# Kernel optimization log

Measured on AMD Instinct MI355X. Metric: run time of the kernel, lower is better.

## Reference

```python
import jax, jax.numpy as jnp
import numpy as np
from jax import lax

B, H_IMG, W_IMG = 512, 812, 40
HID = 128
NUM_CLASSES = 12
LSTM_IN = 32 * ((W_IMG - 5) // 2 + 1)  # 32 channels * 18 = 576


def setup_inputs() -> dict:
    key = jax.random.key(0)
    ks = jax.random.split(key, 20)
    s = 0.05
    inp = {
        "x": jax.random.normal(ks[0], (B, 1, H_IMG, W_IMG), jnp.float32),
        "conv_w": jax.random.normal(ks[1], (32, 1, 20, 5), jnp.float32) * s,
        "conv_b": jax.random.normal(ks[2], (32,), jnp.float32) * s,
        "Wih0": jax.random.normal(ks[3], (4 * HID, LSTM_IN), jnp.float32) * s,
        "Whh0": jax.random.normal(ks[4], (4 * HID, HID), jnp.float32) * s,
        "bih0": jax.random.normal(ks[5], (4 * HID,), jnp.float32) * s,
        "bhh0": jax.random.normal(ks[6], (4 * HID,), jnp.float32) * s,
        "Wih1": jax.random.normal(ks[7], (4 * HID, HID), jnp.float32) * s,
        "Whh1": jax.random.normal(ks[8], (4 * HID, HID), jnp.float32) * s,
        "bih1": jax.random.normal(ks[9], (4 * HID,), jnp.float32) * s,
        "bhh1": jax.random.normal(ks[10], (4 * HID,), jnp.float32) * s,
        "W_att": jax.random.normal(ks[11], (HID, HID), jnp.float32) * s,
        "b_att": jax.random.normal(ks[12], (HID,), jnp.float32) * s,
        "v_att": jax.random.normal(ks[13], (HID,), jnp.float32) * s,
        "W1": jax.random.normal(ks[14], (64, HID), jnp.float32) * s,
        "b1": jax.random.normal(ks[15], (64,), jnp.float32) * s,
        "W2": jax.random.normal(ks[16], (NUM_CLASSES, 64), jnp.float32) * s,
        "b2": jax.random.normal(ks[17], (NUM_CLASSES,), jnp.float32) * s,
    }
    return inp


def _lstm_layer(seq, Wih, Whh, bih, bhh):
    # seq: (T, B, I); PyTorch gate order i, f, g, o
    T, Bn, _ = seq.shape
    Hd = Whh.shape[1]
    x_proj = jnp.einsum('tbi,gi->tbg', seq, Wih) + bih + bhh  # (T,B,4H)

    def step(carry, xg):
        h, c = carry
        g = xg + h @ Whh.T
        i, f, gg, o = jnp.split(g, 4, axis=-1)
        c = jax.nn.sigmoid(f) * c + jax.nn.sigmoid(i) * jnp.tanh(gg)
        h = jax.nn.sigmoid(o) * jnp.tanh(c)
        return (h, c), h

    init = (jnp.zeros((Bn, Hd), seq.dtype), jnp.zeros((Bn, Hd), seq.dtype))
    _, hs = lax.scan(step, init, x_proj)
    return hs  # (T,B,H)


def _forward(x, conv_w, conv_b, Wih0, Whh0, bih0, bhh0, Wih1, Whh1, bih1, bhh1,
             W_att, b_att, v_att, W1, b1, W2, b2):
    # Conv2d(1->32, k=(20,5), s=(8,2)) + ReLU
    y = lax.conv_general_dilated(x, conv_w, (8, 2), 'VALID',
                                 dimension_numbers=('NCHW', 'OIHW', 'NCHW'))
    y = jax.nn.relu(y + conv_b[None, :, None, None])  # (B,32,T,W')
    b, c, t, w = y.shape
    # permute(0,2,3,1).view(b,t,-1).permute(1,0,2) -> (T,B,W'*32)
    seq = jnp.transpose(y, (2, 0, 3, 1)).reshape(t, b, w * c)
    # 2-layer LSTM (inter-layer dropout=0.2 inactive at eval)
    h1 = _lstm_layer(seq, Wih0, Whh0, bih0, bhh0)
    h2 = _lstm_layer(h1, Wih1, Whh1, bih1, bhh1)
    # additive attention pooling over time
    squish = jnp.tanh(jnp.einsum('tbh,hk->tbk', h2, W_att) + b_att)  # (T,B,H)
    attn = jnp.einsum('tbh,h->tb', squish, v_att)                     # (T,B)
    w_att_n = jax.nn.softmax(attn, axis=0)                            # softmax over T
    pooled = jnp.einsum('tb,tbh->bh', w_att_n, h2)                    # (B,H)
    # dnn1 -> (dropout inactive at eval) -> output
    hdn = pooled @ W1.T + b1
    return hdn @ W2.T + b2  # (B,num_classes)


def reference(x, conv_w, conv_b, Wih0, Whh0, bih0, bhh0, Wih1, Whh1, bih1, bhh1,
              W_att, b_att, v_att, W1, b1, W2, b2):
    return _forward(x, conv_w, conv_b, Wih0, Whh0, bih0, bhh0, Wih1, Whh1,
                    bih1, bhh1, W_att, b_att, v_att, W1, b1, W2, b2)
```

## Files before the change

kernel.cpp:

```cpp
#include <hip/hip_runtime.h>
#include <stdint.h>


#define T_STEPS 100
#define BATCH   512
#define HIDD    128
#define GATES   512
#define LSTMIN  576
#define HIMG    812
#define WIMG    40

typedef __attribute__((ext_vector_type(8))) short bf16x8;
typedef __attribute__((ext_vector_type(4))) float f32x4;
typedef __attribute__((ext_vector_type(2))) __fp16 f16x2;

__device__ inline unsigned short f2bf(float f) {
  unsigned u = __float_as_uint(f);
  unsigned r = (u + 0x7fffu + ((u >> 16) & 1u)) >> 16;
  return (unsigned short)r;
}
__device__ inline float bf2f(unsigned short b) {
  return __uint_as_float(((unsigned)b) << 16);
}
__device__ inline float fsigm(float x) {
  float e = __expf(-x);
  return __builtin_amdgcn_rcpf(1.f + e);
}
__device__ inline float ftanh(float x) {
  float e = __expf(2.f * x);
  return (e - 1.f) * __builtin_amdgcn_rcpf(e + 1.f);
}
__device__ inline void lds_barrier() {
  asm volatile("s_waitcnt lgkmcnt(0)" ::: "memory");
  __builtin_amdgcn_s_barrier();
}

__global__ void prep_kernel(const float* __restrict__ Wih0, const float* __restrict__ Whh0,
                            const float* __restrict__ Wih1, const float* __restrict__ Whh1,
                            const float* __restrict__ Watt, const float* __restrict__ convw,
                            const float* __restrict__ bih0, const float* __restrict__ bhh0,
                            const float* __restrict__ bih1, const float* __restrict__ bhh1,
                            unsigned short* __restrict__ wih0b, unsigned short* __restrict__ whh0b,
                            unsigned short* __restrict__ wih1b, unsigned short* __restrict__ whh1b,
                            unsigned short* __restrict__ wattb, f16x2* __restrict__ wpair,
                            float* __restrict__ bias0, float* __restrict__ bias1) {
  int tid = blockIdx.x * blockDim.x + threadIdx.x;
  int stride = gridDim.x * blockDim.x;
  for (int i = tid; i < GATES * LSTMIN; i += stride) wih0b[i] = f2bf(Wih0[i]);
  for (int i = tid; i < GATES * HIDD; i += stride) whh0b[i] = f2bf(Whh0[i]);
  for (int i = tid; i < GATES * HIDD; i += stride) wih1b[i] = f2bf(Wih1[i]);
  for (int i = tid; i < GATES * HIDD; i += stride) whh1b[i] = f2bf(Whh1[i]);
  for (int i = tid; i < HIDD * HIDD; i += stride) {
    int j = i >> 7, k = i & 127;
    wattb[i] = f2bf(Watt[k * HIDD + j]);
  }
  for (int i = tid; i < 50 * 32; i += stride) {
    int k2 = i >> 5, c = i & 31;
    int kh2 = k2 / 5, kw = k2 % 5;
    float lo = convw[c * 100 + (2 * kh2) * 5 + kw];
    float hi = convw[c * 100 + (2 * kh2 + 1) * 5 + kw];
    wpair[i] = __builtin_amdgcn_cvt_pkrtz(lo, hi);
  }
  for (int i = tid; i < GATES; i += stride) bias0[i] = bih0[i] + bhh0[i];
  for (int i = tid; i < GATES; i += stride) bias1[i] = bih1[i] + bhh1[i];
}

__global__ __launch_bounds__(256) void conv_kernel(const float* __restrict__ x,
                                                   const f16x2* __restrict__ wpair,
                                                   const float* __restrict__ convb,
                                                   unsigned short* __restrict__ seq) {
  __shared__ f16x2 imgp[106 * WIMG];
  const int b = blockIdx.x;
  const int chunk = blockIdx.y;
  const int t0 = chunk * 25;
  const float* src = x + (size_t)b * (HIMG * WIMG) + (size_t)(8 * t0) * WIMG;
  for (int i = threadIdx.x; i < 106 * WIMG; i += 256) {
    int r2 = i / WIMG, c = i % WIMG;
    float lo = src[(2 * r2) * WIMG + c];
    float hi = src[(2 * r2 + 1) * WIMG + c];
    imgp[i] = __builtin_amdgcn_cvt_pkrtz(lo, hi);
  }
  __syncthreads();
  for (int p = threadIdx.x; p < 450; p += 256) {
    int tl = p / 18, wp = p % 18;
    int t = t0 + tl;
    float acc[32];
#pragma unroll
    for (int c = 0; c < 32; ++c) acc[c] = 0.f;
    const f16x2* ibase = imgp + (4 * tl) * WIMG + 2 * wp;
#pragma unroll 2
    for (int kh2 = 0; kh2 < 10; ++kh2) {
#pragma unroll
      for (int kw = 0; kw < 5; ++kw) {
        f16x2 iv = ibase[kh2 * WIMG + kw];
        const f16x2* wk = wpair + (kh2 * 5 + kw) * 32;
#pragma unroll
        for (int c = 0; c < 32; ++c)
          acc[c] = __builtin_amdgcn_fdot2(iv, wk[c], acc[c], false);
      }
    }
    unsigned short* o = seq + ((size_t)(t * BATCH + b)) * LSTMIN + wp * 32;
#pragma unroll
    for (int c = 0; c < 32; ++c) {
      float v = acc[c] + convb[c];
      o[c] = f2bf(v > 0.f ? v : 0.f);
    }
  }
}

template <int KDIM>
__global__ __launch_bounds__(256) void gemm_xp_kernel(const unsigned short* __restrict__ A,
                                                      const unsigned short* __restrict__ Bw,
                                                      const float* __restrict__ bias,
                                                      unsigned short* __restrict__ Xp) {
  __shared__ __align__(16) unsigned short As[128 * 32];
  __shared__ __align__(16) unsigned short Bs[128 * 32];
  const int tid = threadIdx.x;
  const int lane = tid & 63;
  const int w = tid >> 6;
  const int col16 = lane & 15;
  const int q = lane >> 4;
  const int n0 = blockIdx.x * 128;
  const int m0 = blockIdx.y * 128;
  const int wm = (w & 1) * 64;
  const int wn = (w >> 1) * 64;
  f32x4 acc[4][4] = {};
  const int r = tid >> 2;
  const int sw = ((tid & 3) ^ (r & 3)) * 8;
  const unsigned wslot = (unsigned)w * 512;
  const unsigned short* ga = A + (size_t)(m0 + r) * KDIM + sw;
  const unsigned short* gb = Bw + (size_t)(n0 + r) * KDIM + sw;
  for (int k0 = 0; k0 < KDIM; k0 += 32) {
    __syncthreads();
    __builtin_amdgcn_global_load_lds((const __attribute__((address_space(1))) void*)(ga + k0),
                                     (__attribute__((address_space(3))) void*)(As + wslot), 16, 0, 0);
    __builtin_amdgcn_global_load_lds((const __attribute__((address_space(1))) void*)(ga + k0 + (size_t)64 * KDIM),
                                     (__attribute__((address_space(3))) void*)(As + wslot + 2048), 16, 0, 0);
    __builtin_amdgcn_global_load_lds((const __attribute__((address_space(1))) void*)(gb + k0),
                                     (__attribute__((address_space(3))) void*)(Bs + wslot), 16, 0, 0);
    __builtin_amdgcn_global_load_lds((const __attribute__((address_space(1))) void*)(gb + k0 + (size_t)64 * KDIM),
                                     (__attribute__((address_space(3))) void*)(Bs + wslot + 2048), 16, 0, 0);
    __syncthreads();
    bf16x8 af[4], bv[4];
#pragma unroll
    for (int i = 0; i < 4; ++i) {
      int ra = wm + i * 16 + col16;
      af[i] = *(const bf16x8*)(As + ra * 32 + ((q ^ (ra & 3)) * 8));
      int rb2 = wn + i * 16 + col16;
      bv[i] = *(const bf16x8*)(Bs + rb2 * 32 + ((q ^ (rb2 & 3)) * 8));
    }
#pragma unroll
    for (int i = 0; i < 4; ++i)
#pragma unroll
      for (int j = 0; j < 4; ++j)
        acc[i][j] = __builtin_amdgcn_mfma_f32_16x16x32_bf16(af[i], bv[j], acc[i][j], 0, 0, 0);
  }
#pragma unroll
  for (int ct = 0; ct < 4; ++ct) {
    int n = n0 + wn + ct * 16 + col16;
    float bvv = bias[n];
    int wS = (n >> 4) & 7;
    int ntS = n >> 7;
    int c16S = n & 15;
#pragma unroll
    for (int rt = 0; rt < 4; ++rt) {
      int m = m0 + wm + rt * 16 + q * 4;
      int t = m >> 9;
      int bb = m & 511;
      int blk = bb >> 4;
      int r16 = bb & 15;
      ushort4 u;
      u.x = f2bf(acc[rt][ct][0] + bvv);
      u.y = f2bf(acc[rt][ct][1] + bvv);
      u.z = f2bf(acc[rt][ct][2] + bvv);
      u.w = f2bf(acc[rt][ct][3] + bvv);
      size_t tile = (((size_t)t * 32 + blk) * 8 + wS) * 4 + ntS;
      *(ushort4*)(Xp + tile * 256 + c16S * 16 + r16) = u;
    }
  }
}

template <bool FUSE_XP, bool WRITE_H>
__global__ __launch_bounds__(512, 2) void scan_kernel(const unsigned short* __restrict__ Xp,
                                                      const unsigned short* __restrict__ Whh,
                                                      const unsigned short* __restrict__ Wih_n,
                                                      const float* __restrict__ bias_n,
                                                      unsigned short* __restrict__ Xp_out,
                                                      unsigned short* __restrict__ hout) {
  __shared__ __align__(16) unsigned short hb[2][16 * 136];
  const int tid = threadIdx.x;
  const int lane = tid & 63;
  const int w = tid >> 6;
  const int col16 = lane & 15;
  const int q = lane >> 4;
  const int rb = blockIdx.x * 16;
  const int blk = blockIdx.x;

  bf16x8 bfrag[4][4];
  bf16x8 bfrag2[4][4];
  const unsigned short* xpb[4];
  unsigned short* xob[4];
  float biasn[4];
#pragma unroll
  for (int nt = 0; nt < 4; ++nt) {
    int cn = nt * HIDD + w * 16 + col16;
#pragma unroll
    for (int ks = 0; ks < 4; ++ks)
      bfrag[nt][ks] = *(const bf16x8*)(Whh + (size_t)cn * HIDD + ks * 32 + q * 8);
    if (FUSE_XP) {
#pragma unroll
      for (int ks = 0; ks < 4; ++ks)
        bfrag2[nt][ks] = *(const bf16x8*)(Wih_n + (size_t)cn * HIDD + ks * 32 + q * 8);
      biasn[nt] = bias_n[cn];
    }
    size_t tile = (((size_t)blk) * 8 + w) * 4 + nt;
    xpb[nt] = Xp + tile * 256 + col16 * 16 + q * 4;
    if (FUSE_XP) xob[nt] = Xp_out + tile * 256 + col16 * 16 + q * 4;
  }
  uint2 xb[2][4];
#pragma unroll
  for (int nt = 0; nt < 4; ++nt) xb[0][nt] = *(const uint2*)(xpb[nt]);
#pragma unroll
  for (int nt = 0; nt < 4; ++nt) xb[1][nt] = *(const uint2*)(xpb[nt] + GATES * BATCH);
  for (int i = tid; i < 2 * 16 * 136; i += 512) hb[0][i] = 0;
  float cst[4] = {0.f, 0.f, 0.f, 0.f};
  lds_barrier();

  const int srow = tid >> 5;
  const int scol = (tid & 31) * 4;
  const int hc = w * 16 + col16;

#pragma unroll 2
  for (int t = 0; t < T_STEPS; ++t) {
    const int pb = (t & 1) ^ 1;
    bf16x8 af[4];
#pragma unroll
    for (int ks = 0; ks < 4; ++ks)
      af[ks] = *(const bf16x8*)(hb[pb] + col16 * 136 + ks * 32 + q * 8);
    if (WRITE_H && t > 0) {
      ushort4 hx = *(const ushort4*)(hb[pb] + srow * 136 + scol);
      *(ushort4*)(hout + ((size_t)((t - 1) * BATCH) + rb + srow) * HIDD + scol) = hx;
    }
    const int s = t & 1;
    uint2 xv[4];
#pragma unroll
    for (int nt = 0; nt < 4; ++nt) xv[nt] = xb[s][nt];
    if (t + 2 < T_STEPS) {
#pragma unroll
      for (int nt = 0; nt < 4; ++nt)
        xb[s][nt] = *(const uint2*)(xpb[nt] + (size_t)(t + 2) * (GATES * BATCH));
    }
    f32x4 acc[4];
#pragma unroll
    for (int nt = 0; nt < 4; ++nt) {
      acc[nt][0] = __uint_as_float(xv[nt].x << 16);
      acc[nt][1] = __uint_as_float(xv[nt].x & 0xffff0000u);
      acc[nt][2] = __uint_as_float(xv[nt].y << 16);
      acc[nt][3] = __uint_as_float(xv[nt].y & 0xffff0000u);
    }
#pragma unroll
    for (int ks = 0; ks < 4; ++ks)
#pragma unroll
      for (int nt = 0; nt < 4; ++nt)
        acc[nt] = __builtin_amdgcn_mfma_f32_16x16x32_bf16(af[ks], bfrag[nt][ks], acc[nt], 0, 0, 0);
    f32x4 acc2[4];
    if (FUSE_XP) {
#pragma unroll
      for (int nt = 0; nt < 4; ++nt) acc2[nt] = f32x4{0.f, 0.f, 0.f, 0.f};
#pragma unroll
      for (int ks = 0; ks < 4; ++ks)
#pragma unroll
        for (int nt = 0; nt < 4; ++nt)
          acc2[nt] = __builtin_amdgcn_mfma_f32_16x16x32_bf16(af[ks], bfrag2[nt][ks], acc2[nt], 0, 0, 0);
    }
    unsigned short hv[4];
#pragma unroll
    for (int rr = 0; rr < 4; ++rr) {
      float pi = acc[0][rr], pf = acc[1][rr];
      float pg = acc[2][rr], po = acc[3][rr];
      float cc = fsigm(pf) * cst[rr] + fsigm(pi) * ftanh(pg);
      cst[rr] = cc;
      hv[rr] = f2bf(fsigm(po) * ftanh(cc));
    }
    if (FUSE_XP) {
      if (t > 0) {
#pragma unroll
        for (int nt = 0; nt < 4; ++nt) {
          ushort4 u;
          u.x = f2bf(acc2[nt][0] + biasn[nt]);
          u.y = f2bf(acc2[nt][1] + biasn[nt]);
          u.z = f2bf(acc2[nt][2] + biasn[nt]);
          u.w = f2bf(acc2[nt][3] + biasn[nt]);
          *(ushort4*)(xob[nt] + (size_t)(t - 1) * (GATES * BATCH)) = u;
        }
      }
    }
#pragma unroll
    for (int rr = 0; rr < 4; ++rr)
      hb[t & 1][(q * 4 + rr) * 136 + hc] = hv[rr];
    lds_barrier();
  }
  if (WRITE_H) {
    ushort4 hx = *(const ushort4*)(hb[(T_STEPS - 1) & 1] + srow * 136 + scol);
    *(ushort4*)(hout + ((size_t)((T_STEPS - 1) * BATCH) + rb + srow) * HIDD + scol) = hx;
  }
  if (FUSE_XP) {
    bf16x8 af[4];
#pragma unroll
    for (int ks = 0; ks < 4; ++ks)
      af[ks] = *(const bf16x8*)(hb[(T_STEPS - 1) & 1] + col16 * 136 + ks * 32 + q * 8);
    f32x4 acc2[4];
#pragma unroll
    for (int nt = 0; nt < 4; ++nt) acc2[nt] = f32x4{0.f, 0.f, 0.f, 0.f};
#pragma unroll
    for (int ks = 0; ks < 4; ++ks)
#pragma unroll
      for (int nt = 0; nt < 4; ++nt)
        acc2[nt] = __builtin_amdgcn_mfma_f32_16x16x32_bf16(af[ks], bfrag2[nt][ks], acc2[nt], 0, 0, 0);
#pragma unroll
    for (int nt = 0; nt < 4; ++nt) {
      ushort4 u;
      u.x = f2bf(acc2[nt][0] + biasn[nt]);
      u.y = f2bf(acc2[nt][1] + biasn[nt]);
      u.z = f2bf(acc2[nt][2] + biasn[nt]);
      u.w = f2bf(acc2[nt][3] + biasn[nt]);
      *(ushort4*)(xob[nt] + (size_t)(T_STEPS - 1) * (GATES * BATCH)) = u;
    }
  }
}

__global__ __launch_bounds__(256) void gemm_att_kernel(const unsigned short* __restrict__ A,
                                                       const unsigned short* __restrict__ Bw,
                                                       const float* __restrict__ b_att,
                                                       const float* __restrict__ v_att,
                                                       float* __restrict__ scores) {
  __shared__ __align__(16) unsigned short As[128 * 32];
  __shared__ __align__(16) unsigned short Bs[128 * 32];
  __shared__ float s_red[128];
  const int tid = threadIdx.x;
  const int lane = tid & 63;
  const int w = tid >> 6;
  const int col16 = lane & 15;
  const int q = lane >> 4;
  const int m0 = blockIdx.y * 128;
  const int wm = (w & 1) * 64;
  const int wn = (w >> 1) * 64;
  f32x4 acc[4][4] = {};
  const int r = tid >> 2;
  const int sw = ((tid & 3) ^ (r & 3)) * 8;
  const unsigned wslot = (unsigned)w * 512;
  const unsigned short* ga = A + (size_t)(m0 + r) * HIDD + sw;
  const unsigned short* gb = Bw + (size_t)r * HIDD + sw;
  for (int k0 = 0; k0 < HIDD; k0 += 32) {
    __syncthreads();
    __builtin_amdgcn_global_load_lds((const __attribute__((address_space(1))) void*)(ga + k0),
                                     (__attribute__((address_space(3))) void*)(As + wslot), 16, 0, 0);
    __builtin_amdgcn_global_load_lds((const __attribute__((address_space(1))) void*)(ga + k0 + (size_t)64 * HIDD),
                                     (__attribute__((address_space(3))) void*)(As + wslot + 2048), 16, 0, 0);
    __builtin_amdgcn_global_load_lds((const __attribute__((address_space(1))) void*)(gb + k0),
                                     (__attribute__((address_space(3))) void*)(Bs + wslot), 16, 0, 0);
    __builtin_amdgcn_global_load_lds((const __attribute__((address_space(1))) void*)(gb + k0 + (size_t)64 * HIDD),
                                     (__attribute__((address_space(3))) void*)(Bs + wslot + 2048), 16, 0, 0);
    __syncthreads();
    bf16x8 af[4], bv[4];
#pragma unroll
    for (int i = 0; i < 4; ++i) {
      int ra = wm + i * 16 + col16;
      af[i] = *(const bf16x8*)(As + ra * 32 + ((q ^ (ra & 3)) * 8));
      int rb2 = wn + i * 16 + col16;
      bv[i] = *(const bf16x8*)(Bs + rb2 * 32 + ((q ^ (rb2 & 3)) * 8));
    }
#pragma unroll
    for (int i = 0; i < 4; ++i)
#pragma unroll
      for (int j = 0; j < 4; ++j)
        acc[i][j] = __builtin_amdgcn_mfma_f32_16x16x32_bf16(af[i], bv[j], acc[i][j], 0, 0, 0);
  }
  if (tid < 128) s_red[tid] = 0.f;
  float rs[4][4];
#pragma unroll
  for (int rt = 0; rt < 4; ++rt)
#pragma unroll
    for (int rr = 0; rr < 4; ++rr) rs[rt][rr] = 0.f;
#pragma unroll
  for (int ct = 0; ct < 4; ++ct) {
    int n = wn + ct * 16 + col16;
    float bvv = b_att[n], vv = v_att[n];
#pragma unroll
    for (int rt = 0; rt < 4; ++rt)
#pragma unroll
      for (int rr = 0; rr < 4; ++rr) {
        float xv2 = acc[rt][ct][rr] + bvv;
        float e = __expf(2.f * xv2);
        rs[rt][rr] += vv * (e - 1.f) * __builtin_amdgcn_rcpf(e + 1.f);
      }
  }
#pragma unroll
  for (int off = 1; off < 16; off <<= 1)
#pragma unroll
    for (int rt = 0; rt < 4; ++rt)
#pragma unroll
      for (int rr = 0; rr < 4; ++rr) rs[rt][rr] += __shfl_xor(rs[rt][rr], off, 64);
  __syncthreads();
  if (col16 == 0) {
#pragma unroll
    for (int rt = 0; rt < 4; ++rt)
#pragma unroll
      for (int rr = 0; rr < 4; ++rr)
        atomicAdd(&s_red[wm + rt * 16 + q * 4 + rr], rs[rt][rr]);
  }
  __syncthreads();
  if (tid < 128) scores[m0 + tid] = s_red[tid];
}

__global__ __launch_bounds__(128) void final_kernel(const float* __restrict__ scores,
                                                    const unsigned short* __restrict__ h2,
                                                    const float* __restrict__ W1, const float* __restrict__ b1,
                                                    const float* __restrict__ W2, const float* __restrict__ b2,
                                                    float* __restrict__ out) {
  const int b = blockIdx.x;
  const int tid = threadIdx.x;
  __shared__ float wj[T_STEPS];
  __shared__ float red[128];
  __shared__ float pooled[128];
  __shared__ float hdn[64];
  float sv = (tid < T_STEPS) ? scores[tid * BATCH + b] : -1e30f;
  red[tid] = sv;
  __syncthreads();
#pragma unroll
  for (int off = 64; off > 0; off >>= 1) {
    if (tid < off) red[tid] = fmaxf(red[tid], red[tid + off]);
    __syncthreads();
  }
  float mx = red[0];
  __syncthreads();
  float ev = (tid < T_STEPS) ? __expf(sv - mx) : 0.f;
  red[tid] = ev;
  __syncthreads();
#pragma unroll
  for (int off = 64; off > 0; off >>= 1) {
    if (tid < off) red[tid] += red[tid + off];
    __syncthreads();
  }
  float inv = 1.0f / red[0];
  if (tid < T_STEPS) wj[tid] = ev * inv;
  __syncthreads();
  float p = 0.f;
  for (int t = 0; t < T_STEPS; ++t)
    p += wj[t] * bf2f(h2[((size_t)(t * BATCH + b)) * HIDD + tid]);
  pooled[tid] = p;
  __syncthreads();
  if (tid < 64) {
    float a = b1[tid];
    for (int h = 0; h < 128; ++h) a = fmaf(W1[tid * 128 + h], pooled[h], a);
    hdn[tid] = a;
  }
  __syncthreads();
  if (tid < 12) {
    float a = b2[tid];
    for (int j = 0; j < 64; ++j) a = fmaf(W2[tid * 64 + j], hdn[j], a);
    out[b * 12 + tid] = a;
  }
}

extern "C" void kernel_launch(void* const* d_in, const int* in_sizes, int n_in,
                              void* d_out, int out_size, void* d_ws, size_t ws_size,
                              hipStream_t stream) {
  (void)in_sizes; (void)n_in; (void)out_size; (void)ws_size;
  const float* x      = (const float*)d_in[0];
  const float* conv_w = (const float*)d_in[1];
  const float* conv_b = (const float*)d_in[2];
  const float* Wih0   = (const float*)d_in[3];
  const float* Whh0   = (const float*)d_in[4];
  const float* bih0   = (const float*)d_in[5];
  const float* bhh0   = (const float*)d_in[6];
  const float* Wih1   = (const float*)d_in[7];
  const float* Whh1   = (const float*)d_in[8];
  const float* bih1   = (const float*)d_in[9];
  const float* bhh1   = (const float*)d_in[10];
  const float* W_att  = (const float*)d_in[11];
  const float* b_att  = (const float*)d_in[12];
  const float* v_att  = (const float*)d_in[13];
  const float* W1     = (const float*)d_in[14];
  const float* b1     = (const float*)d_in[15];
  const float* W2     = (const float*)d_in[16];
  const float* b2     = (const float*)d_in[17];

  char* ws = (char*)d_ws;
  size_t off = 0;
  auto carve = [&](size_t bytes) { char* p = ws + off; off += (bytes + 255) & ~(size_t)255; return p; };
  unsigned short* seq    = (unsigned short*)carve((size_t)T_STEPS * BATCH * LSTMIN * 2);
  unsigned short* xp0    = (unsigned short*)carve((size_t)T_STEPS * GATES * BATCH * 2);
  unsigned short* h2     = (unsigned short*)carve((size_t)T_STEPS * BATCH * HIDD * 2);
  float*          scores = (float*)carve((size_t)T_STEPS * BATCH * 4);
  unsigned short* wih0b  = (unsigned short*)carve((size_t)GATES * LSTMIN * 2);
  unsigned short* whh0b  = (unsigned short*)carve((size_t)GATES * HIDD * 2);
  unsigned short* wih1b  = (unsigned short*)carve((size_t)GATES * HIDD * 2);
  unsigned short* whh1b  = (unsigned short*)carve((size_t)GATES * HIDD * 2);
  unsigned short* wattb  = (unsigned short*)carve((size_t)HIDD * HIDD * 2);
  f16x2*          wpair  = (f16x2*)carve(50 * 32 * 4);
  float*          bias0  = (float*)carve(GATES * 4);
  float*          bias1  = (float*)carve(GATES * 4);
  unsigned short* xp1 = seq;

  prep_kernel<<<256, 256, 0, stream>>>(Wih0, Whh0, Wih1, Whh1, W_att, conv_w,
                                       bih0, bhh0, bih1, bhh1,
                                       wih0b, whh0b, wih1b, whh1b, wattb, wpair, bias0, bias1);
  conv_kernel<<<dim3(512, 4), 256, 0, stream>>>(x, wpair, conv_b, seq);
  gemm_xp_kernel<LSTMIN><<<dim3(4, 400), 256, 0, stream>>>(seq, wih0b, bias0, xp0);
  scan_kernel<true, false><<<32, 512, 0, stream>>>(xp0, whh0b, wih1b, bias1, xp1, nullptr);
  scan_kernel<false, true><<<32, 512, 0, stream>>>(xp1, whh1b, nullptr, nullptr, nullptr, h2);
  gemm_att_kernel<<<dim3(1, 400), 256, 0, stream>>>(h2, wattb, b_att, v_att, scores);
  final_kernel<<<512, 128, 0, stream>>>(scores, h2, W1, b1, W2, b2, (float*)d_out);
}
```

Baseline: 500.8 us.

## Pipeline both LSTM layer scans in one kernel with flag-based producer/consumer sync

Replaces the two back-to-back scan launches with a single 64-block kernel. Blocks 0-31 run layer 0 and emit layer-1 input projections, and blocks 32-63 run layer 1 a few timesteps behind. Consumers poll per-batch-tile global flags that producers publish with release stores every four steps. This lets the two latency-bound recurrences overlap instead of running serially. The cost is polling, extra full barriers in the producer, and reliance on all 64 blocks being resident at once and on cross-XCD memory visibility.

```diff
diff --git a/kernel.cpp b/kernel.cpp
--- a/kernel.cpp
+++ b/kernel.cpp
@@ -33,6 +33,19 @@
 __device__ inline void lds_barrier() {
   asm volatile("s_waitcnt lgkmcnt(0)" ::: "memory");
   __builtin_amdgcn_s_barrier();
+}
+__device__ inline void full_barrier() {
+  asm volatile("s_waitcnt vmcnt(0) lgkmcnt(0)" ::: "memory");
+  __builtin_amdgcn_s_barrier();
+}
+__device__ inline void wait_flag(const int* fp, int need) {
+  if ((threadIdx.x & 63) == 0) {
+    int v = __hip_atomic_load(fp, __ATOMIC_ACQUIRE, __HIP_MEMORY_SCOPE_AGENT);
+    while (v < need) {
+      __builtin_amdgcn_s_sleep(2);
+      v = __hip_atomic_load(fp, __ATOMIC_ACQUIRE, __HIP_MEMORY_SCOPE_AGENT);
+    }
+  }
 }
 
 __global__ void prep_kernel(const float* __restrict__ Wih0, const float* __restrict__ Whh0,
@@ -43,7 +56,8 @@
                             unsigned short* __restrict__ wih0b, unsigned short* __restrict__ whh0b,
                             unsigned short* __restrict__ wih1b, unsigned short* __restrict__ whh1b,
                             unsigned short* __restrict__ wattb, f16x2* __restrict__ wpair,
-                            float* __restrict__ bias0, float* __restrict__ bias1) {
+                            float* __restrict__ bias0, float* __restrict__ bias1,
+                            int* __restrict__ flags) {
   int tid = blockIdx.x * blockDim.x + threadIdx.x;
   int stride = gridDim.x * blockDim.x;
   for (int i = tid; i < GATES * LSTMIN; i += stride) wih0b[i] = f2bf(Wih0[i]);
@@ -63,6 +77,7 @@
   }
   for (int i = tid; i < GATES; i += stride) bias0[i] = bih0[i] + bhh0[i];
   for (int i = tid; i < GATES; i += stride) bias1[i] = bih1[i] + bhh1[i];
+  for (int i = tid; i < 32; i += stride) flags[i] = 0;
 }
 
 __global__ __launch_bounds__(256) void conv_kernel(const float* __restrict__ x,
@@ -180,91 +195,82 @@
   }
 }
 
-template <bool FUSE_XP, bool WRITE_H>
-__global__ __launch_bounds__(512, 2) void scan_kernel(const unsigned short* __restrict__ Xp,
-                                                      const unsigned short* __restrict__ Whh,
-                                                      const unsigned short* __restrict__ Wih_n,
-                                                      const float* __restrict__ bias_n,
-                                                      unsigned short* __restrict__ Xp_out,
-                                                      unsigned short* __restrict__ hout) {
+__global__ __launch_bounds__(512, 2) void scan_pipe_kernel(
+    const unsigned short* __restrict__ Xp0, const unsigned short* __restrict__ Whh0,
+    const unsigned short* __restrict__ Wih1, const float* __restrict__ bias1,
+    unsigned short* __restrict__ Xp1, const unsigned short* __restrict__ Whh1,
+    unsigned short* __restrict__ hout, int* __restrict__ flags) {
   __shared__ __align__(16) unsigned short hb[2][16 * 136];
   const int tid = threadIdx.x;
   const int lane = tid & 63;
   const int w = tid >> 6;
   const int col16 = lane & 15;
   const int q = lane >> 4;
-  const int rb = blockIdx.x * 16;
-  const int blk = blockIdx.x;
-
-  bf16x8 bfrag[4][4];
-  bf16x8 bfrag2[4][4];
-  const unsigned short* xpb[4];
-  unsigned short* xob[4];
-  float biasn[4];
-#pragma unroll
-  for (int nt = 0; nt < 4; ++nt) {
-    int cn = nt * HIDD + w * 16 + col16;
-#pragma unroll
-    for (int ks = 0; ks < 4; ++ks)
-      bfrag[nt][ks] = *(const bf16x8*)(Whh + (size_t)cn * HIDD + ks * 32 + q * 8);
-    if (FUSE_XP) {
-#pragma unroll
-      for (int ks = 0; ks < 4; ++ks)
-        bfrag2[nt][ks] = *(const bf16x8*)(Wih_n + (size_t)cn * HIDD + ks * 32 + q * 8);
-      biasn[nt] = bias_n[cn];
-    }
-    size_t tile = (((size_t)blk) * 8 + w) * 4 + nt;
-    xpb[nt] = Xp + tile * 256 + col16 * 16 + q * 4;
-    if (FUSE_XP) xob[nt] = Xp_out + tile * 256 + col16 * 16 + q * 4;
-  }
-  uint2 xb[2][4];
-#pragma unroll
-  for (int nt = 0; nt < 4; ++nt) xb[0][nt] = *(const uint2*)(xpb[nt]);
-#pragma unroll
-  for (int nt = 0; nt < 4; ++nt) xb[1][nt] = *(const uint2*)(xpb[nt] + GATES * BATCH);
-  for (int i = tid; i < 2 * 16 * 136; i += 512) hb[0][i] = 0;
-  float cst[4] = {0.f, 0.f, 0.f, 0.f};
-  lds_barrier();
-
+  const bool producer = blockIdx.x < 32;
+  const int blk = producer ? (int)blockIdx.x : (int)blockIdx.x - 32;
+  const int rb = blk * 16;
+  const int hc = w * 16 + col16;
   const int srow = tid >> 5;
   const int scol = (tid & 31) * 4;
-  const int hc = w * 16 + col16;
-
-#pragma unroll 2
-  for (int t = 0; t < T_STEPS; ++t) {
-    const int pb = (t & 1) ^ 1;
-    bf16x8 af[4];
-#pragma unroll
-    for (int ks = 0; ks < 4; ++ks)
-      af[ks] = *(const bf16x8*)(hb[pb] + col16 * 136 + ks * 32 + q * 8);
-    if (WRITE_H && t > 0) {
-      ushort4 hx = *(const ushort4*)(hb[pb] + srow * 136 + scol);
-      *(ushort4*)(hout + ((size_t)((t - 1) * BATCH) + rb + srow) * HIDD + scol) = hx;
-    }
-    const int s = t & 1;
-    uint2 xv[4];
-#pragma unroll
-    for (int nt = 0; nt < 4; ++nt) xv[nt] = xb[s][nt];
-    if (t + 2 < T_STEPS) {
-#pragma unroll
-      for (int nt = 0; nt < 4; ++nt)
-        xb[s][nt] = *(const uint2*)(xpb[nt] + (size_t)(t + 2) * (GATES * BATCH));
-    }
-    f32x4 acc[4];
+  int* flagp = flags + blk;
+
+  if (producer) {
+    bf16x8 bfrag[4][4], bfrag2[4][4];
+    const unsigned short* xpb[4];
+    unsigned short* xob[4];
+    float biasn[4];
 #pragma unroll
     for (int nt = 0; nt < 4; ++nt) {
-      acc[nt][0] = __uint_as_float(xv[nt].x << 16);
-      acc[nt][1] = __uint_as_float(xv[nt].x & 0xffff0000u);
-      acc[nt][2] = __uint_as_float(xv[nt].y << 16);
-      acc[nt][3] = __uint_as_float(xv[nt].y & 0xffff0000u);
-    }
-#pragma unroll
-    for (int ks = 0; ks < 4; ++ks)
-#pragma unroll
-      for (int nt = 0; nt < 4; ++nt)
-        acc[nt] = __builtin_amdgcn_mfma_f32_16x16x32_bf16(af[ks], bfrag[nt][ks], acc[nt], 0, 0, 0);
-    f32x4 acc2[4];
-    if (FUSE_XP) {
+      int cn = nt * HIDD + hc;
+#pragma unroll
+      for (int ks = 0; ks < 4; ++ks) {
+        bfrag[nt][ks] = *(const bf16x8*)(Whh0 + (size_t)cn * HIDD + ks * 32 + q * 8);
+        bfrag2[nt][ks] = *(const bf16x8*)(Wih1 + (size_t)cn * HIDD + ks * 32 + q * 8);
+      }
+      biasn[nt] = bias1[cn];
+      size_t tile = (((size_t)blk) * 8 + w) * 4 + nt;
+      xpb[nt] = Xp0 + tile * 256 + col16 * 16 + q * 4;
+      xob[nt] = Xp1 + tile * 256 + col16 * 16 + q * 4;
+    }
+    uint2 xb[2][4];
+#pragma unroll
+    for (int nt = 0; nt < 4; ++nt) xb[0][nt] = *(const uint2*)(xpb[nt]);
+#pragma unroll
+    for (int nt = 0; nt < 4; ++nt) xb[1][nt] = *(const uint2*)(xpb[nt] + GATES * BATCH);
+    for (int i = tid; i < 2 * 16 * 136; i += 512) hb[0][i] = 0;
+    float cst[4] = {0.f, 0.f, 0.f, 0.f};
+    lds_barrier();
+
+#pragma unroll 4
+    for (int t = 0; t < T_STEPS; ++t) {
+      const int pb = (t & 1) ^ 1;
+      bf16x8 af[4];
+#pragma unroll
+      for (int ks = 0; ks < 4; ++ks)
+        af[ks] = *(const bf16x8*)(hb[pb] + col16 * 136 + ks * 32 + q * 8);
+      const int s = t & 1;
+      uint2 xv[4];
+#pragma unroll
+      for (int nt = 0; nt < 4; ++nt) xv[nt] = xb[s][nt];
+      if (t + 2 < T_STEPS) {
+#pragma unroll
+        for (int nt = 0; nt < 4; ++nt)
+          xb[s][nt] = *(const uint2*)(xpb[nt] + (size_t)(t + 2) * (GATES * BATCH));
+      }
+      f32x4 acc[4];
+#pragma unroll
+      for (int nt = 0; nt < 4; ++nt) {
+        acc[nt][0] = __uint_as_float(xv[nt].x << 16);
+        acc[nt][1] = __uint_as_float(xv[nt].x & 0xffff0000u);
+        acc[nt][2] = __uint_as_float(xv[nt].y << 16);
+        acc[nt][3] = __uint_as_float(xv[nt].y & 0xffff0000u);
+      }
+#pragma unroll
+      for (int ks = 0; ks < 4; ++ks)
+#pragma unroll
+        for (int nt = 0; nt < 4; ++nt)
+          acc[nt] = __builtin_amdgcn_mfma_f32_16x16x32_bf16(af[ks], bfrag[nt][ks], acc[nt], 0, 0, 0);
+      f32x4 acc2[4];
 #pragma unroll
       for (int nt = 0; nt < 4; ++nt) acc2[nt] = f32x4{0.f, 0.f, 0.f, 0.f};
 #pragma unroll
@@ -272,17 +278,15 @@
 #pragma unroll
         for (int nt = 0; nt < 4; ++nt)
           acc2[nt] = __builtin_amdgcn_mfma_f32_16x16x32_bf16(af[ks], bfrag2[nt][ks], acc2[nt], 0, 0, 0);
-    }
-    unsigned short hv[4];
-#pragma unroll
-    for (int rr = 0; rr < 4; ++rr) {
-      float pi = acc[0][rr], pf = acc[1][rr];
-      float pg = acc[2][rr], po = acc[3][rr];
-      float cc = fsigm(pf) * cst[rr] + fsigm(pi) * ftanh(pg);
-      cst[rr] = cc;
-      hv[rr] = f2bf(fsigm(po) * ftanh(cc));
-    }
-    if (FUSE_XP) {
+      unsigned short hv[4];
+#pragma unroll
+      for (int rr = 0; rr < 4; ++rr) {
+        float pi = acc[0][rr], pf = acc[1][rr];
+        float pg = acc[2][rr], po = acc[3][rr];
+        float cc = fsigm(pf) * cst[rr] + fsigm(pi) * ftanh(pg);
+        cst[rr] = cc;
+        hv[rr] = f2bf(fsigm(po) * ftanh(cc));
+      }
       if (t > 0) {
 #pragma unroll
         for (int nt = 0; nt < 4; ++nt) {
@@ -294,17 +298,17 @@
           *(ushort4*)(xob[nt] + (size_t)(t - 1) * (GATES * BATCH)) = u;
         }
       }
-    }
-#pragma unroll
-    for (int rr = 0; rr < 4; ++rr)
-      hb[t & 1][(q * 4 + rr) * 136 + hc] = hv[rr];
-    lds_barrier();
-  }
-  if (WRITE_H) {
-    ushort4 hx = *(const ushort4*)(hb[(T_STEPS - 1) & 1] + srow * 136 + scol);
-    *(ushort4*)(hout + ((size_t)((T_STEPS - 1) * BATCH) + rb + srow) * HIDD + scol) = hx;
-  }
-  if (FUSE_XP) {
+#pragma unroll
+      for (int rr = 0; rr < 4; ++rr)
+        hb[t & 1][(q * 4 + rr) * 136 + hc] = hv[rr];
+      if ((t & 3) == 3) {
+        full_barrier();
+        if (tid == 0)
+          __hip_atomic_store(flagp, t, __ATOMIC_RELEASE, __HIP_MEMORY_SCOPE_AGENT);
+      } else {
+        lds_barrier();
+      }
+    }
     bf16x8 af[4];
 #pragma unroll
     for (int ks = 0; ks < 4; ++ks)
@@ -326,6 +330,85 @@
       u.w = f2bf(acc2[nt][3] + biasn[nt]);
       *(ushort4*)(xob[nt] + (size_t)(T_STEPS - 1) * (GATES * BATCH)) = u;
     }
+    full_barrier();
+    if (tid == 0)
+      __hip_atomic_store(flagp, 100, __ATOMIC_RELEASE, __HIP_MEMORY_SCOPE_AGENT);
+  } else {
+    bf16x8 bfrag[4][4];
+    const unsigned short* xpb[4];
+#pragma unroll
+    for (int nt = 0; nt < 4; ++nt) {
+      int cn = nt * HIDD + hc;
+#pragma unroll
+      for (int ks = 0; ks < 4; ++ks)
+        bfrag[nt][ks] = *(const bf16x8*)(Whh1 + (size_t)cn * HIDD + ks * 32 + q * 8);
+      size_t tile = (((size_t)blk) * 8 + w) * 4 + nt;
+      xpb[nt] = Xp1 + tile * 256 + col16 * 16 + q * 4;
+    }
+    for (int i = tid; i < 2 * 16 * 136; i += 512) hb[0][i] = 0;
+    wait_flag(flagp, 6);
+    uint2 xb[2][4];
+#pragma unroll
+    for (int nt = 0; nt < 4; ++nt) xb[0][nt] = *(const uint2*)(xpb[nt]);
+#pragma unroll
+    for (int nt = 0; nt < 4; ++nt) xb[1][nt] = *(const uint2*)(xpb[nt] + GATES * BATCH);
+    float cst[4] = {0.f, 0.f, 0.f, 0.f};
+    lds_barrier();
+
+#pragma unroll 4
+    for (int t = 0; t < T_STEPS; ++t) {
+      if (t > 0 && (t & 3) == 0) {
+        int need = t + 6;
+        if (need > 100) need = 100;
+        wait_flag(flagp, need);
+      }
+      const int pb = (t & 1) ^ 1;
+      bf16x8 af[4];
+#pragma unroll
+      for (int ks = 0; ks < 4; ++ks)
+        af[ks] = *(const bf16x8*)(hb[pb] + col16 * 136 + ks * 32 + q * 8);
+      if (t > 0) {
+        ushort4 hx = *(const ushort4*)(hb[pb] + srow * 136 + scol);
+        *(ushort4*)(hout + ((size_t)((t - 1) * BATCH) + rb + srow) * HIDD + scol) = hx;
+      }
+      const int s = t & 1;
+      uint2 xv[4];
+#pragma unroll
+      for (int nt = 0; nt < 4; ++nt) xv[nt] = xb[s][nt];
+      if (t + 2 < T_STEPS) {
+#pragma unroll
+        for (int nt = 0; nt < 4; ++nt)
+          xb[s][nt] = *(const uint2*)(xpb[nt] + (size_t)(t + 2) * (GATES * BATCH));
+      }
+      f32x4 acc[4];
+#pragma unroll
+      for (int nt = 0; nt < 4; ++nt) {
+        acc[nt][0] = __uint_as_float(xv[nt].x << 16);
+        acc[nt][1] = __uint_as_float(xv[nt].x & 0xffff0000u);
+        acc[nt][2] = __uint_as_float(xv[nt].y << 16);
+        acc[nt][3] = __uint_as_float(xv[nt].y & 0xffff0000u);
+      }
+#pragma unroll
+      for (int ks = 0; ks < 4; ++ks)
+#pragma unroll
+        for (int nt = 0; nt < 4; ++nt)
+          acc[nt] = __builtin_amdgcn_mfma_f32_16x16x32_bf16(af[ks], bfrag[nt][ks], acc[nt], 0, 0, 0);
+      unsigned short hv[4];
+#pragma unroll
+      for (int rr = 0; rr < 4; ++rr) {
+        float pi = acc[0][rr], pf = acc[1][rr];
+        float pg = acc[2][rr], po = acc[3][rr];
+        float cc = fsigm(pf) * cst[rr] + fsigm(pi) * ftanh(pg);
+        cst[rr] = cc;
+        hv[rr] = f2bf(fsigm(po) * ftanh(cc));
+      }
+#pragma unroll
+      for (int rr = 0; rr < 4; ++rr)
+        hb[t & 1][(q * 4 + rr) * 136 + hc] = hv[rr];
+      lds_barrier();
+    }
+    ushort4 hx = *(const ushort4*)(hb[(T_STEPS - 1) & 1] + srow * 136 + scol);
+    *(ushort4*)(hout + ((size_t)((T_STEPS - 1) * BATCH) + rb + srow) * HIDD + scol) = hx;
   }
 }
 
@@ -501,15 +584,16 @@
   f16x2*          wpair  = (f16x2*)carve(50 * 32 * 4);
   float*          bias0  = (float*)carve(GATES * 4);
   float*          bias1  = (float*)carve(GATES * 4);
+  int*            flags  = (int*)carve(32 * 4);
   unsigned short* xp1 = seq;
 
   prep_kernel<<<256, 256, 0, stream>>>(Wih0, Whh0, Wih1, Whh1, W_att, conv_w,
                                        bih0, bhh0, bih1, bhh1,
-                                       wih0b, whh0b, wih1b, whh1b, wattb, wpair, bias0, bias1);
+                                       wih0b, whh0b, wih1b, whh1b, wattb, wpair,
+                                       bias0, bias1, flags);
   conv_kernel<<<dim3(512, 4), 256, 0, stream>>>(x, wpair, conv_b, seq);
   gemm_xp_kernel<LSTMIN><<<dim3(4, 400), 256, 0, stream>>>(seq, wih0b, bias0, xp0);
-  scan_kernel<true, false><<<32, 512, 0, stream>>>(xp0, whh0b, wih1b, bias1, xp1, nullptr);
-  scan_kernel<false, true><<<32, 512, 0, stream>>>(xp1, whh1b, nullptr, nullptr, nullptr, h2);
+  scan_pipe_kernel<<<64, 512, 0, stream>>>(xp0, whh0b, wih1b, bias1, xp1, whh1b, h2, flags);
   gemm_att_kernel<<<dim3(1, 400), 256, 0, stream>>>(h2, wattb, b_att, v_att, scores);
   final_kernel<<<512, 128, 0, stream>>>(scores, h2, W1, b1, W2, b2, (float*)d_out);
 }
```

Measured after the change: 412.5 us. -17.6%, faster.
